# Kernel tuning notes

Measured on AMD Instinct MI355X. Metric: run time of the kernel, lower is better.

Reference implementation:

```python
import jax, jax.numpy as jnp
import numpy as np

TOTAL = 67108864      # flat length of values
N_SEG = 1048576       # number of jagged segments


def setup_inputs() -> dict:
    key = jax.random.key(0)
    k1, k2 = jax.random.split(key)
    values = jax.random.normal(k1, (TOTAL,), dtype=jnp.float32)
    # cumulative end-offsets: sorted, strictly within (0, TOTAL], last pinned to TOTAL
    prefix_sum = jnp.sort(jax.random.randint(k2, (N_SEG,), 1, TOTAL, dtype=jnp.int64))
    prefix_sum = prefix_sum.at[-1].set(TOTAL)
    return {"values": values, "prefix_sum": prefix_sum}


def reference(values, prefix_sum):
    """Jagged per-segment argmax.

    values: [total] flat concatenation of segments.
    prefix_sum: [n_seg] cumulative end offsets (prefix_sum[-1] == total).
    Returns: [n_seg] int32 global flat index of the (first) max element in
    each segment. Empty segments (duplicate offsets) get sentinel `total`.
    """
    total = values.shape[0]
    n_seg = prefix_sum.shape[0]
    pos = jnp.arange(total, dtype=jnp.int32)
    # element i belongs to the first segment whose end offset exceeds i
    ids = jnp.searchsorted(prefix_sum, pos, side="right")  # [total]
    # per-segment max value
    maxv = jax.ops.segment_max(values, ids, num_segments=n_seg)  # [n_seg]
    # first global index attaining the segment max
    cand = jnp.where(values == maxv[ids], pos, total)
    idx = jax.ops.segment_min(cand, ids, num_segments=n_seg)  # [n_seg]
    return idx
```

## Files before the change

kernel.cpp:

```cpp
#include <hip/hip_runtime.h>
#include <cstdint>


#define IMAX      0x7FFFFFFF
#define C_CHUNK   4096
#define CAP       240
#define INIT_PACK 0x007FFFFF00000000ull
#define NEG_INF   __int_as_float(0xFF800000u)

__device__ __forceinline__ unsigned long long pack_vi(float v, int idx) {
    unsigned u = __float_as_uint(v);
    u = (u & 0x80000000u) ? ~u : (u | 0x80000000u);
    return ((unsigned long long)u << 32) |
           (unsigned long long)(0xFFFFFFFFu - (unsigned)idx);
}
__device__ __forceinline__ int decode_idx(unsigned long long p) {
    if (p == INIT_PACK) return IMAX;
    return (int)(0xFFFFFFFFu - (unsigned)(p & 0xFFFFFFFFull));
}

template<int CTRL>
__device__ __forceinline__ float dpp_fmax(float v) {
    int moved = __builtin_amdgcn_update_dpp((int)0xFF800000, __float_as_int(v),
                                            CTRL, 0xF, 0xF, false);
    return fmaxf(v, __int_as_float(moved));
}
template<int CTRL>
__device__ __forceinline__ int dpp_imin(int v) {
    int moved = __builtin_amdgcn_update_dpp(IMAX, v, CTRL, 0xF, 0xF, false);
    return min(v, moved);
}
__device__ __forceinline__ int wave_argmax64(float bv, int bi) {
    float m = bv;
    m = dpp_fmax<0xB1>(m); m = dpp_fmax<0x4E>(m);
    m = dpp_fmax<0x124>(m); m = dpp_fmax<0x128>(m);
    float r0 = __int_as_float(__builtin_amdgcn_readlane(__float_as_int(m), 0));
    float r1 = __int_as_float(__builtin_amdgcn_readlane(__float_as_int(m), 16));
    float r2 = __int_as_float(__builtin_amdgcn_readlane(__float_as_int(m), 32));
    float r3 = __int_as_float(__builtin_amdgcn_readlane(__float_as_int(m), 48));
    float maxv = fmaxf(fmaxf(r0, r1), fmaxf(r2, r3));
    int cand = (bv == maxv) ? bi : IMAX;
    cand = dpp_imin<0xB1>(cand); cand = dpp_imin<0x4E>(cand);
    cand = dpp_imin<0x124>(cand); cand = dpp_imin<0x128>(cand);
    int i0 = __builtin_amdgcn_readlane(cand, 0);
    int i1 = __builtin_amdgcn_readlane(cand, 16);
    int i2 = __builtin_amdgcn_readlane(cand, 32);
    int i3 = __builtin_amdgcn_readlane(cand, 48);
    return min(min(i0, i1), min(i2, i3));
}

__global__ void chunk_starts_kernel(const int* __restrict__ ps32, int n_seg,
                                    int nchunks, int2* __restrict__ cs) {
    int c = blockIdx.x * blockDim.x + threadIdx.x;
    if (c >= nchunks) return;
    const bool is64 = (ps32[1] == 0);
    const long long* ps64 = (const long long*)ps32;
    long long c0 = (long long)c * C_CHUNK;
    int lo = 0, hi = n_seg;
    while (lo < hi) {
        int mid = (lo + hi) >> 1;
        long long b = is64 ? ps64[mid] : (long long)ps32[mid];
        if (b > c0) hi = mid; else lo = mid + 1;
    }
    int start0 = lo ? (int)(is64 ? ps64[lo - 1] : (long long)ps32[lo - 1]) : 0;
    cs[c] = make_int2(lo, start0);
}

__global__ __launch_bounds__(256) void jagged_main_kernel(
    const float* __restrict__ values,
    const int*   __restrict__ ps32,
    int n_seg,
    int* __restrict__ out,
    const int2* __restrict__ cs)
{
    __shared__ int lds_ps[CAP + 1];
    __shared__ unsigned long long lds_res[CAP];
    __shared__ int sh_span;

    const int tid = (int)threadIdx.x;
    const int c0 = (int)blockIdx.x * C_CHUNK;
    const int chunkEnd = c0 + C_CHUNK;
    const int w = tid >> 6, l = tid & 63;

    const int mybase = c0 + (tid << 4);
    const float4* vp = (const float4*)(values + mybase);
    float4 e0 = vp[0], e1 = vp[1], e2 = vp[2], e3 = vp[3];

    const int2 sw = cs[blockIdx.x];
    const int s0 = sw.x, start0 = sw.y;

    const bool is64 = (ps32[1] == 0);
    const long long* ps64 = (const long long*)ps32;

    if (tid < CAP) {
        int s = s0 + tid;
        lds_ps[tid] = (s < n_seg) ? (int)(is64 ? ps64[s] : (long long)ps32[s])
                                  : IMAX;
        lds_res[tid] = INIT_PACK;
    }
    if (tid == 0) { lds_ps[CAP] = IMAX; sh_span = -1; }
    __syncthreads();

    int lo = 0, hi = CAP;
    while (lo < hi) {
        int mid = (lo + hi) >> 1;
        if (lds_ps[mid] > mybase) hi = mid; else lo = mid + 1;
    }
    int j = lo;
    int bnd = lds_ps[j];
    float bv = NEG_INF;
    int   bi = IMAX;

#define PROC_ELEM(VV, OFF)                                              \
    {                                                                   \
        int idx = mybase + (OFF);                                       \
        float v = (VV);                                                 \
        while (idx >= bnd) {                                            \
            if (bi != IMAX)                                             \
                atomicMax(&lds_res[min(j, CAP - 1)], pack_vi(bv, bi));  \
            bv = NEG_INF; bi = IMAX;                                    \
            ++j; bnd = lds_ps[min(j, CAP)];                             \
        }                                                               \
        if (v > bv) { bv = v; bi = idx; }                               \
    }
#define PROC4(R, E)                                                     \
    PROC_ELEM((E).x, (R)*4 + 0) PROC_ELEM((E).y, (R)*4 + 1)             \
    PROC_ELEM((E).z, (R)*4 + 2) PROC_ELEM((E).w, (R)*4 + 3)
    PROC4(0, e0) PROC4(1, e1) PROC4(2, e2) PROC4(3, e3)
#undef PROC4
#undef PROC_ELEM
    if (bi != IMAX) atomicMax(&lds_res[min(j, CAP - 1)], pack_vi(bv, bi));
    __syncthreads();

    if (tid < CAP) {
        int s = s0 + tid;
        if (s < n_seg) {
            int end_b   = lds_ps[tid];
            int start_b = tid ? lds_ps[tid - 1] : start0;
            if (start_b == end_b) {
                if (start_b > c0 && start_b <= chunkEnd) out[s] = IMAX;
            } else if (start_b >= c0 && start_b < chunkEnd) {
                if (end_b <= chunkEnd) out[s] = decode_idx(lds_res[tid]);
                else sh_span = tid;
            }
        }
    }
    __syncthreads();

    const int span = sh_span;
    if (span >= 0 && w == 0) {
        int end_b   = lds_ps[span];
        int start_b = span ? lds_ps[span - 1] : start0;
        float sv = NEG_INF; int si = IMAX;
        for (int i = start_b + l; i < end_b; i += 64) {
            float v = values[i];
            if (v > sv) { sv = v; si = i; }
        }
        int idx = wave_argmax64(sv, si);
        if (l == 0) out[s0 + span] = idx;
    }
}

__device__ __forceinline__ void upd_pair(const float* __restrict__ values,
                                         int i, int end, float& bv, int& bi) {
    float v0 = (i     < end) ? values[i]     : NEG_INF;
    float v1 = (i + 1 < end) ? values[i + 1] : NEG_INF;
    if (v0 > bv) { bv = v0; bi = i; }
    if (v1 > bv) { bv = v1; bi = i + 1; }
}
__global__ __launch_bounds__(256) void jagged_fallback_kernel(
    const float* __restrict__ values, const int* __restrict__ ps32,
    int n_seg, int* __restrict__ out)
{
    const int pair = blockIdx.x * (blockDim.x >> 6) + ((int)threadIdx.x >> 6);
    const int lane = (int)threadIdx.x & 63;
    const int seg0 = pair * 2;
    if (seg0 >= n_seg) return;
    const bool has1 = (seg0 + 1) < n_seg;
    const bool is64 = (ps32[1] == 0);
    const long long* ps64 = (const long long*)ps32;
    int s0, e0, e1;
    if (is64) { s0 = seg0 ? (int)ps64[seg0-1] : 0; e0 = (int)ps64[seg0];
                e1 = has1 ? (int)ps64[seg0+1] : e0; }
    else      { s0 = seg0 ? ps32[seg0-1] : 0; e0 = ps32[seg0];
                e1 = has1 ? ps32[seg0+1] : e0; }
    float bv0 = NEG_INF, bv1 = NEG_INF; int bi0 = IMAX, bi1 = IMAX;
    upd_pair(values, s0 + 2*lane, e0, bv0, bi0);
    upd_pair(values, e0 + 2*lane, e1, bv1, bi1);
    for (int i = s0 + 2*lane + 128; i < e0; i += 128) upd_pair(values, i, e0, bv0, bi0);
    for (int i = e0 + 2*lane + 128; i < e1; i += 128) upd_pair(values, i, e1, bv1, bi1);
    int idx0 = wave_argmax64(bv0, bi0);
    int idx1 = wave_argmax64(bv1, bi1);
    int myi = (lane == 0) ? idx0 : idx1;
    if (lane < (has1 ? 2 : 1)) out[seg0 + lane] = myi;
}

extern "C" void kernel_launch(void* const* d_in, const int* in_sizes, int n_in,
                              void* d_out, int out_size, void* d_ws, size_t ws_size,
                              hipStream_t stream) {
    const float* values = (const float*)d_in[0];
    const int*   ps32   = (const int*)d_in[1];
    const int n_seg = in_sizes[1];
    const int total = in_sizes[0];
    int* out = (int*)d_out;

    const int nchunks = total / C_CHUNK;
    if ((total % C_CHUNK) == 0 && ws_size >= (size_t)nchunks * sizeof(int2)) {
        int2* cs = (int2*)d_ws;
        chunk_starts_kernel<<<(nchunks + 255) / 256, 256, 0, stream>>>(
            ps32, n_seg, nchunks, cs);
        jagged_main_kernel<<<nchunks, 256, 0, stream>>>(
            values, ps32, n_seg, out, cs);
    } else {
        const int segs_per_block = 8;
        const int grid = (n_seg + segs_per_block - 1) / segs_per_block;
        jagged_fallback_kernel<<<grid, 256, 0, stream>>>(values, ps32, n_seg, out);
    }
}
```

Baseline: 61.41 us.

## Fuse chunk-start search into main kernel via wave-parallel 64-ary search

Removes the separate chunk_starts kernel launch and its workspace round-trip. Each wave in the main kernel now finds the chunk's first segment itself, using a 64-way ballot search over prefix_sum that needs about four rounds for a million segments. The cost is that every block, and all four waves within it, repeats this search with global loads. The 64-bit case is handled by reading only the low 32-bit words.

```diff
diff --git a/kernel.cpp b/kernel.cpp
--- a/kernel.cpp
+++ b/kernel.cpp
@@ -49,29 +49,11 @@
     return min(min(i0, i1), min(i2, i3));
 }
 
-__global__ void chunk_starts_kernel(const int* __restrict__ ps32, int n_seg,
-                                    int nchunks, int2* __restrict__ cs) {
-    int c = blockIdx.x * blockDim.x + threadIdx.x;
-    if (c >= nchunks) return;
-    const bool is64 = (ps32[1] == 0);
-    const long long* ps64 = (const long long*)ps32;
-    long long c0 = (long long)c * C_CHUNK;
-    int lo = 0, hi = n_seg;
-    while (lo < hi) {
-        int mid = (lo + hi) >> 1;
-        long long b = is64 ? ps64[mid] : (long long)ps32[mid];
-        if (b > c0) hi = mid; else lo = mid + 1;
-    }
-    int start0 = lo ? (int)(is64 ? ps64[lo - 1] : (long long)ps32[lo - 1]) : 0;
-    cs[c] = make_int2(lo, start0);
-}
-
 __global__ __launch_bounds__(256) void jagged_main_kernel(
     const float* __restrict__ values,
     const int*   __restrict__ ps32,
     int n_seg,
-    int* __restrict__ out,
-    const int2* __restrict__ cs)
+    int* __restrict__ out)
 {
     __shared__ int lds_ps[CAP + 1];
     __shared__ unsigned long long lds_res[CAP];
@@ -86,27 +68,38 @@
     const float4* vp = (const float4*)(values + mybase);
     float4 e0 = vp[0], e1 = vp[1], e2 = vp[2], e3 = vp[3];
 
-    const int2 sw = cs[blockIdx.x];
-    const int s0 = sw.x, start0 = sw.y;
-
     const bool is64 = (ps32[1] == 0);
-    const long long* ps64 = (const long long*)ps32;
+    const int  psw  = is64 ? 2 : 1;
+    int lo = 0, hi = n_seg - 1;
+    while (lo < hi) {
+        int step = (hi - lo + 63) >> 6;
+        int pos  = lo + l * step;
+        int posc = min(pos, hi);
+        bool cond = (ps32[posc * psw] > c0);
+        unsigned long long m = __ballot(cond);
+        if (m == 0) { lo = lo + 63 * step + 1; continue; }
+        int f = (int)__builtin_ctzll(m);
+        if (f == 0) { hi = lo; break; }
+        hi = min(lo + f * step, hi);
+        lo = lo + (f - 1) * step + 1;
+    }
+    const int s0 = lo;
+    const int start0 = s0 ? ps32[(s0 - 1) * psw] : 0;
 
     if (tid < CAP) {
         int s = s0 + tid;
-        lds_ps[tid] = (s < n_seg) ? (int)(is64 ? ps64[s] : (long long)ps32[s])
-                                  : IMAX;
+        lds_ps[tid]  = (s < n_seg) ? ps32[s * psw] : IMAX;
         lds_res[tid] = INIT_PACK;
     }
     if (tid == 0) { lds_ps[CAP] = IMAX; sh_span = -1; }
     __syncthreads();
 
-    int lo = 0, hi = CAP;
-    while (lo < hi) {
-        int mid = (lo + hi) >> 1;
-        if (lds_ps[mid] > mybase) hi = mid; else lo = mid + 1;
-    }
-    int j = lo;
+    int blo = 0, bhi = CAP;
+    while (blo < bhi) {
+        int mid = (blo + bhi) >> 1;
+        if (lds_ps[mid] > mybase) bhi = mid; else blo = mid + 1;
+    }
+    int j = blo;
     int bnd = lds_ps[j];
     float bv = NEG_INF;
     int   bi = IMAX;
@@ -204,13 +197,9 @@
     const int total = in_sizes[0];
     int* out = (int*)d_out;
 
-    const int nchunks = total / C_CHUNK;
-    if ((total % C_CHUNK) == 0 && ws_size >= (size_t)nchunks * sizeof(int2)) {
-        int2* cs = (int2*)d_ws;
-        chunk_starts_kernel<<<(nchunks + 255) / 256, 256, 0, stream>>>(
-            ps32, n_seg, nchunks, cs);
-        jagged_main_kernel<<<nchunks, 256, 0, stream>>>(
-            values, ps32, n_seg, out, cs);
+    if ((total % C_CHUNK) == 0 && n_seg >= 2) {
+        const int nchunks = total / C_CHUNK;
+        jagged_main_kernel<<<nchunks, 256, 0, stream>>>(values, ps32, n_seg, out);
     } else {
         const int segs_per_block = 8;
         const int grid = (n_seg + segs_per_block - 1) / segs_per_block;
```

After: 72.56 us. 1.18x slower.
